# Performance work log

Measured on AMD Instinct MI355X. Metric: run time of the kernel, lower is better.

Reference implementation:

```python
import jax, jax.numpy as jnp
import numpy as np

B, T, D, H = 32, 1024, 512, 256  # bidirectional: hidden per direction = d_model // 2


def setup_inputs() -> dict:
    key = jax.random.key(0)
    ks = jax.random.split(key, 9)
    s = 1.0 / np.sqrt(H)  # torch default init scale
    return {
        "x": jax.random.normal(ks[0], (B, T, D), jnp.float32),
        "Wih_f": jax.random.normal(ks[1], (4 * H, D), jnp.float32) * s,
        "Whh_f": jax.random.normal(ks[2], (4 * H, H), jnp.float32) * s,
        "bih_f": jax.random.normal(ks[3], (4 * H,), jnp.float32) * s,
        "bhh_f": jax.random.normal(ks[4], (4 * H,), jnp.float32) * s,
        "Wih_b": jax.random.normal(ks[5], (4 * H, D), jnp.float32) * s,
        "Whh_b": jax.random.normal(ks[6], (4 * H, H), jnp.float32) * s,
        "bib_b": jax.random.normal(ks[7], (4 * H,), jnp.float32) * s,
        "bhh_b": jax.random.normal(ks[8], (4 * H,), jnp.float32) * s,
    }


def _lstm_dir(x, Wih, Whh, bih, bhh):
    # x: [B, T, D]; torch gate order: i, f, g, o
    b, t, _ = x.shape
    h_dim = Whh.shape[1]
    xp = jnp.einsum('btd,gd->btg', x, Wih) + bih + bhh  # [B, T, 4H]

    def step(carry, xt):
        h, c = carry
        gates = xt + h @ Whh.T  # [B, 4H]
        i, f, g, o = jnp.split(gates, 4, axis=-1)
        i = jax.nn.sigmoid(i)
        f = jax.nn.sigmoid(f)
        g = jnp.tanh(g)
        o = jax.nn.sigmoid(o)
        c = f * c + i * g
        h = o * jnp.tanh(c)
        return (h, c), h

    init = (jnp.zeros((b, h_dim), x.dtype), jnp.zeros((b, h_dim), x.dtype))
    _, hs = jax.lax.scan(step, init, jnp.swapaxes(xp, 0, 1))  # [T, B, H]
    return jnp.swapaxes(hs, 0, 1)  # [B, T, H]


def reference(x, Wih_f, Whh_f, bih_f, bhh_f, Wih_b, Whh_b, bib_b, bhh_b):
    # force_1d is identity for 3D input
    out_f = _lstm_dir(x, Wih_f, Whh_f, bih_f, bhh_f)
    out_b = _lstm_dir(x[:, ::-1, :], Wih_b, Whh_b, bib_b, bhh_b)[:, ::-1, :]
    return jnp.concatenate([out_f, out_b], axis=-1)  # [B, T, 2H] = [B, T, d_model]
```

## Files before the change

### kernel.cpp

```cpp
#include <hip/hip_runtime.h>
#include <cstdint>
#include <cstddef>


typedef unsigned int   uint;
typedef unsigned short ushort;

constexpr int Tn = 1024;
constexpr int Bn = 32;
constexpr int Dn = 512;
constexpr int Hn = 256;
constexpr int NC = 2048;
constexpr int KT = 512;

typedef _Float16 half8  __attribute__((ext_vector_type(8)));
typedef float    f32x4  __attribute__((ext_vector_type(4)));
typedef int      i32x4  __attribute__((ext_vector_type(4)));

__device__ __forceinline__ ushort f2h(float f) {
  _Float16 h = (_Float16)f;
  return __builtin_bit_cast(ushort, h);
}
__device__ __forceinline__ float h2f(ushort s) {
  return (float)__builtin_bit_cast(_Float16, s);
}
__device__ __forceinline__ uint packh(float a, float b) {
  return (uint)f2h(a) | ((uint)f2h(b) << 16);
}
__device__ __forceinline__ f32x4 mf(uint4 a, uint4 b, f32x4 c) {
  return __builtin_amdgcn_mfma_f32_16x16x32_f16(
      __builtin_bit_cast(half8, a), __builtin_bit_cast(half8, b), c, 0, 0, 0);
}
__device__ __forceinline__ i32x4 mfi8(uint4 a, uint4 b, i32x4 c) {
  return __builtin_amdgcn_mfma_i32_16x16x64_i8(
      __builtin_bit_cast(i32x4, a), __builtin_bit_cast(i32x4, b), c, 0, 0, 0);
}

__device__ __forceinline__ float sig_(float x) {
  x = fminf(fmaxf(x, -30.f), 30.f);
  return 1.f / (1.f + __expf(-x));
}
__device__ __forceinline__ float tanh_(float x) {
  x = fminf(fmaxf(x, -15.f), 15.f);
  float e = __expf(2.f * x);
  return (e - 1.f) / (e + 1.f);
}

__device__ __forceinline__ void barrier_lgkm() {
  asm volatile("s_waitcnt lgkmcnt(0)" ::: "memory");
  __builtin_amdgcn_s_barrier();
}


__global__ void k_prep_a(const float* __restrict__ x, ushort* __restrict__ a16, long nquad) {
  long i4 = (long)blockIdx.x * blockDim.x + threadIdx.x;
  if (i4 >= nquad) return;
  const float4 v = ((const float4*)x)[i4];
  ushort4 o;
  o.x = f2h(v.x); o.y = f2h(v.y); o.z = f2h(v.z); o.w = f2h(v.w);
  ((ushort4*)a16)[i4] = o;
}

__global__ void k_prep_w(const float* __restrict__ wf, const float* __restrict__ wb,
                         const float* __restrict__ bf1, const float* __restrict__ bf2,
                         const float* __restrict__ bb1, const float* __restrict__ bb2,
                         ushort* __restrict__ w16, float* __restrict__ biasc) {
  long i4 = (long)blockIdx.x * blockDim.x + threadIdx.x;
  if (i4 >= (long)NC * (KT / 4)) return;
  int n = (int)(i4 >> 7);
  int k4 = (int)(i4 & 127);
  int dir = n >> 10, g = n & 1023;
  const float* w = dir ? wb : wf;
  const float4 v = ((const float4*)(w + (size_t)g * Dn))[k4];
  ushort4 o;
  o.x = f2h(v.x); o.y = f2h(v.y); o.z = f2h(v.z); o.w = f2h(v.w);
  ((ushort4*)w16)[i4] = o;
  if (k4 == 0) biasc[n] = dir ? (bb1[g] + bb2[g]) : (bf1[g] + bf2[g]);
}

__global__ void k_scale(const float* __restrict__ whhF, const float* __restrict__ whhB,
                        float* __restrict__ sq) {
  int t = blockIdx.x * blockDim.x + threadIdx.x;
  if (t >= 2048) return;
  int dir = t >> 10, row = t & 1023;
  const float* w = (dir ? whhB : whhF) + (size_t)row * Hn;
  float m = 0.f;
  for (int i = 0; i < Hn; ++i) m = fmaxf(m, fabsf(w[i]));
  sq[t] = fmaxf(m, 1e-30f) / 127.f;
}

__global__ void k_prep_whh8(const float* __restrict__ whhF, const float* __restrict__ whhB,
                            const float* __restrict__ sq, uint4* __restrict__ WF8) {
  int t = blockIdx.x * blockDim.x + threadIdx.x;
  if (t >= 2 * 8 * 32 * 64) return;
  int lane = t & 63;
  int frag = (t >> 6) & 31;
  int w    = (t >> 11) & 7;
  int dir  = (t >> 14) & 1;
  int m  = frag & 7, kt = frag >> 3;
  int g = m >> 1, j = m & 1;
  int row = (g * 16 + 2 * w + j) * 16 + (lane & 15);
  int kb  = kt * 64 + (lane >> 4) * 16;
  const float* whh = dir ? whhB : whhF;
  const float* src = whh + (size_t)row * Hn + kb;
  float inv = 1.f / sq[dir * 1024 + row];
  uint pk[4];
#pragma unroll
  for (int q = 0; q < 4; ++q) {
    uint v = 0;
#pragma unroll
    for (int b = 0; b < 4; ++b) {
      float f = src[q * 4 + b] * inv;
      int iq = (int)rintf(fminf(fmaxf(f, -127.f), 127.f));
      v |= ((uint)(unsigned char)(signed char)iq) << (8 * b);
    }
    pk[q] = v;
  }
  WF8[t] = (uint4){pk[0], pk[1], pk[2], pk[3]};
}

__global__ void k_bad(float* __restrict__ out, int n) {
  int i = blockIdx.x * blockDim.x + threadIdx.x;
  if (i < n) out[i] = 54321.f;
}


__device__ __forceinline__ void gload_lds16(const void* g, void* l) {
  __builtin_amdgcn_global_load_lds((const __attribute__((address_space(1))) void*)g,
                                   (__attribute__((address_space(3))) void*)l, 16, 0, 0);
}

__global__ __launch_bounds__(256) void k_gemm(const ushort* __restrict__ A,
                                              const ushort* __restrict__ W,
                                              const float* __restrict__ biasc,
                                              ushort* __restrict__ xp) {
  __shared__ __align__(16) ushort As[128 * 32];
  __shared__ __align__(16) ushort Bs[128 * 32];
  const int bid = blockIdx.x;
  const int m0 = (bid >> 4) * 128;
  const int n0 = (bid & 15) * 128;
  const int tid = threadIdx.x;
  const int wid = tid >> 6, lane = tid & 63;
  const int wr = wid >> 1, wcq = wid & 1;
  const int l16 = lane & 15, lq = lane >> 4;

  f32x4 acc[4][4] = {};

  for (int kt = 0; kt < KT; kt += 32) {
    __syncthreads();
#pragma unroll
    for (int i = 0; i < 2; ++i) {
      int ch = wid * 2 + i;
      int p = ch * 64 + lane;
      int r = p >> 2, gp = p & 3;
      int gs = gp ^ ((r >> 1) & 3);
      gload_lds16(A + (size_t)(m0 + r) * KT + kt + gs * 8, (char*)As + ch * 1024);
      gload_lds16(W + (size_t)(n0 + r) * KT + kt + gs * 8, (char*)Bs + ch * 1024);
    }
    __syncthreads();

    half8 af[4], bfr[4];
#pragma unroll
    for (int mfi = 0; mfi < 4; ++mfi) {
      int row = wr * 64 + mfi * 16 + l16;
      int g = lq ^ ((row >> 1) & 3);
      af[mfi] = *(const half8*)((const char*)As + row * 64 + g * 16);
    }
#pragma unroll
    for (int nf = 0; nf < 4; ++nf) {
      int row = wcq * 64 + nf * 16 + l16;
      int g = lq ^ ((row >> 1) & 3);
      bfr[nf] = *(const half8*)((const char*)Bs + row * 64 + g * 16);
    }
#pragma unroll
    for (int mfi = 0; mfi < 4; ++mfi)
#pragma unroll
      for (int nf = 0; nf < 4; ++nf)
        acc[mfi][nf] = __builtin_amdgcn_mfma_f32_16x16x32_f16(af[mfi], bfr[nf], acc[mfi][nf], 0, 0, 0);
  }

#pragma unroll
  for (int nf = 0; nf < 4; ++nf) {
    int col = n0 + wcq * 64 + nf * 16 + l16;
    float bv = biasc[col];
#pragma unroll
    for (int mfi = 0; mfi < 4; ++mfi) {
      int rbase = m0 + wr * 64 + mfi * 16 + lq * 4;
#pragma unroll
      for (int i = 0; i < 4; ++i)
        xp[(size_t)(rbase + i) * NC + col] = f2h(acc[mfi][nf][i] + bv);
    }
  }
}


__global__ __launch_bounds__(512, 2) void k_lstm(const uint4* __restrict__ WF8,
                                                 const float* __restrict__ sq,
                                                 const ushort* __restrict__ xp,
                                                 float* __restrict__ out,
                                                 int b_base) {
  const int dir = blockIdx.x & 1;
  const int bl  = blockIdx.x >> 1;
  const int tid = threadIdx.x;
  const int w    = tid >> 6;
  const int lane = tid & 63;
  const int lq   = lane >> 4;
  const int n    = lane & 31;

  __shared__ __align__(16) char hq[2][256];
  __shared__ __align__(16) int  gbuf[8][128];

  const uint4* wfb = WF8 + (size_t)((dir * 8 + w) * 32) * 64 + lane;
  uint4 wA[32];
#pragma unroll
  for (int f = 0; f < 32; ++f) wA[f] = wfb[(size_t)f * 64];

  float fdq[4];
#pragma unroll
  for (int g = 0; g < 4; ++g)
    fdq[g] = sq[dir * 1024 + g * 256 + 32 * w + n] * (1.f / 127.f);

  if (tid < 128) ((uint*)hq)[tid] = 0;
  float creg = 0.f;
  __syncthreads();

  const int dstep = dir ? -1 : 1;
  const int t0 = dir ? (Tn - 1) : 0;
  const ptrdiff_t xstr = (ptrdiff_t)dstep * NC;
  const ptrdiff_t ostr = (ptrdiff_t)dstep * 512;
  const ushort* px = xp + (size_t)(bl * Tn + t0) * NC + dir * 1024 + 32 * w + n;
  float* pout = out + (size_t)((b_base + bl) * Tn + t0) * 512 + dir * 256 + 32 * w + n;

  int cur = 0;
#pragma unroll 1
  for (int t = 0; t < Tn; ++t) {
    ushort xg0 = px[0], xg1 = px[256], xg2 = px[512], xg3 = px[768];
    px += xstr;

    uint4 bq[4];
#pragma unroll
    for (int kt = 0; kt < 4; ++kt)
      bq[kt] = *(const uint4*)(hq[cur] + kt * 64 + lq * 16);

    i32x4 acc[8];
#pragma unroll
    for (int m = 0; m < 8; ++m) acc[m] = (i32x4){0, 0, 0, 0};
#pragma unroll
    for (int kt = 0; kt < 4; ++kt)
#pragma unroll
      for (int m = 0; m < 8; ++m)
        acc[m] = mfi8(wA[kt * 8 + m], bq[kt], acc[m]);

    if ((lane & 15) == 0) {
#pragma unroll
      for (int m = 0; m < 8; ++m)
        *(i32x4*)&gbuf[w][(m >> 1) * 32 + (m & 1) * 16 + lq * 4] = acc[m];
    }
    float gi = (float)gbuf[w][0 * 32 + n] * fdq[0] + h2f(xg0);
    float gf = (float)gbuf[w][1 * 32 + n] * fdq[1] + h2f(xg1);
    float gg = (float)gbuf[w][2 * 32 + n] * fdq[2] + h2f(xg2);
    float go = (float)gbuf[w][3 * 32 + n] * fdq[3] + h2f(xg3);
    float iv = sig_(gi), fv = sig_(gf), gv = tanh_(gg), ov = sig_(go);
    creg = fv * creg + iv * gv;
    float h = ov * tanh_(creg);
    if (lane < 32) {
      *pout = h;
      int q = (int)rintf(h * 127.f);
      hq[cur ^ 1][32 * w + n] = (char)q;
    }
    pout += ostr;
    barrier_lgkm();
    cur ^= 1;
  }
}


extern "C" void kernel_launch(void* const* d_in, const int* in_sizes, int n_in,
                              void* d_out, int out_size, void* d_ws, size_t ws_size,
                              hipStream_t stream) {
  const float* x     = (const float*)d_in[0];
  const float* Wih_f = (const float*)d_in[1];
  const float* Whh_f = (const float*)d_in[2];
  const float* bih_f = (const float*)d_in[3];
  const float* bhh_f = (const float*)d_in[4];
  const float* Wih_b = (const float*)d_in[5];
  const float* Whh_b = (const float*)d_in[6];
  const float* bib_b = (const float*)d_in[7];
  const float* bhh_b = (const float*)d_in[8];
  float* out = (float*)d_out;

  const size_t szW16  = (size_t)NC * KT * 2;
  const size_t szBias = (size_t)NC * 4;
  const size_t szSq   = 2048 * 4;
  const size_t szWF8  = (size_t)2 * 8 * 32 * 64 * 16;

  int c = 0;
  size_t szA16 = 0, szXp = 0;
  for (int cc = 1; cc <= 16; cc *= 2) {
    size_t a = (size_t)(Bn / cc) * Tn * KT * 2;
    size_t p = (size_t)(Bn / cc) * Tn * NC * 2;
    if (szW16 + szBias + szSq + szWF8 + a + p <= ws_size) { c = cc; szA16 = a; szXp = p; break; }
  }
  if (c == 0) {
    k_bad<<<(out_size + 255) / 256, 256, 0, stream>>>(out, out_size);
    return;
  }

  char* ws = (char*)d_ws;
  ushort* W16   = (ushort*)ws;
  float*  biasc = (float*)(ws + szW16);
  float*  sq    = (float*)(ws + szW16 + szBias);
  uint4*  WF8   = (uint4*)(ws + szW16 + szBias + szSq);
  ushort* A16   = (ushort*)(ws + szW16 + szBias + szSq + szWF8);
  ushort* xp    = (ushort*)(ws + szW16 + szBias + szSq + szWF8 + szA16);

  {
    long n4 = (long)NC * (KT / 4);
    k_prep_w<<<(int)((n4 + 255) / 256), 256, 0, stream>>>(Wih_f, Wih_b, bih_f, bhh_f,
                                                          bib_b, bhh_b, W16, biasc);
  }
  k_scale<<<8, 256, 0, stream>>>(Whh_f, Whh_b, sq);
  k_prep_whh8<<<(2 * 8 * 32 * 64) / 256, 256, 0, stream>>>(Whh_f, Whh_b, sq, WF8);

  const int sizeB = Bn / c;
  for (int cb = 0; cb < c; ++cb) {
    const int b_base = cb * sizeB;
    {
      long nquad = (long)sizeB * Tn * KT / 4;
      k_prep_a<<<(int)((nquad + 255) / 256), 256, 0, stream>>>(
          x + (size_t)b_base * Tn * Dn, A16, nquad);
    }
    k_gemm<<<dim3(sizeB * 8 * 16), dim3(256), 0, stream>>>(A16, W16, biasc, xp);
    k_lstm<<<dim3(2 * sizeB), dim3(512), 0, stream>>>(WF8, sq, xp, out, b_base);
  }
}
```

Before: 1.307 ms.

## Prefetch next-step xp gates, split MFMA chains, use fast reciprocal activations

Loads the next timestep's input-projection values one iteration ahead so their global-load latency overlaps the current step's recurrent MFMA work. It also splits the eight MFMA accumulators into two interleaved halves, storing the even half to LDS before issuing the odd half. Sigmoid and tanh now use a hardware reciprocal builtin without clamping. This trims latency on the serial per-timestep critical path, at the cost of slightly lower activation precision and possible inf handling at extreme inputs.

```diff
diff --git a/kernel.cpp b/kernel.cpp
--- a/kernel.cpp
+++ b/kernel.cpp
@@ -36,14 +36,25 @@
       __builtin_bit_cast(i32x4, a), __builtin_bit_cast(i32x4, b), c, 0, 0, 0);
 }
 
+#if defined(__has_builtin)
+#  if __has_builtin(__builtin_amdgcn_rcpf)
+#    define RCPF(x) __builtin_amdgcn_rcpf(x)
+#  endif
+#endif
+#ifndef RCPF
+#  define RCPF(x) (1.f / (x))
+#endif
+
+__device__ __forceinline__ float sigr_(float x) {
+  return RCPF(1.f + __expf(-x));
+}
+__device__ __forceinline__ float tanhr_(float x) {
+  float e = __expf(2.f * x);
+  return fmaf(-2.f, RCPF(e + 1.f), 1.f);
+}
 __device__ __forceinline__ float sig_(float x) {
   x = fminf(fmaxf(x, -30.f), 30.f);
   return 1.f / (1.f + __expf(-x));
-}
-__device__ __forceinline__ float tanh_(float x) {
-  x = fminf(fmaxf(x, -15.f), 15.f);
-  float e = __expf(2.f * x);
-  return (e - 1.f) / (e + 1.f);
 }
 
 __device__ __forceinline__ void barrier_lgkm() {
@@ -231,47 +242,65 @@
   const ushort* px = xp + (size_t)(bl * Tn + t0) * NC + dir * 1024 + 32 * w + n;
   float* pout = out + (size_t)((b_base + bl) * Tn + t0) * 512 + dir * 256 + 32 * w + n;
 
+  float xc0 = h2f(px[0]), xc1 = h2f(px[256]), xc2 = h2f(px[512]), xc3 = h2f(px[768]);
+
   int cur = 0;
 #pragma unroll 1
   for (int t = 0; t < Tn; ++t) {
-    ushort xg0 = px[0], xg1 = px[256], xg2 = px[512], xg3 = px[768];
-    px += xstr;
-
     uint4 bq[4];
 #pragma unroll
     for (int kt = 0; kt < 4; ++kt)
       bq[kt] = *(const uint4*)(hq[cur] + kt * 64 + lq * 16);
 
+    float xn0 = 0.f, xn1 = 0.f, xn2 = 0.f, xn3 = 0.f;
+    if (t + 1 < Tn) {
+      px += xstr;
+      xn0 = h2f(px[0]); xn1 = h2f(px[256]); xn2 = h2f(px[512]); xn3 = h2f(px[768]);
+    }
+
     i32x4 acc[8];
 #pragma unroll
     for (int m = 0; m < 8; ++m) acc[m] = (i32x4){0, 0, 0, 0};
+
 #pragma unroll
     for (int kt = 0; kt < 4; ++kt)
 #pragma unroll
-      for (int m = 0; m < 8; ++m)
+      for (int m = 0; m < 8; m += 2)
         acc[m] = mfi8(wA[kt * 8 + m], bq[kt], acc[m]);
-
     if ((lane & 15) == 0) {
 #pragma unroll
-      for (int m = 0; m < 8; ++m)
-        *(i32x4*)&gbuf[w][(m >> 1) * 32 + (m & 1) * 16 + lq * 4] = acc[m];
-    }
-    float gi = (float)gbuf[w][0 * 32 + n] * fdq[0] + h2f(xg0);
-    float gf = (float)gbuf[w][1 * 32 + n] * fdq[1] + h2f(xg1);
-    float gg = (float)gbuf[w][2 * 32 + n] * fdq[2] + h2f(xg2);
-    float go = (float)gbuf[w][3 * 32 + n] * fdq[3] + h2f(xg3);
-    float iv = sig_(gi), fv = sig_(gf), gv = tanh_(gg), ov = sig_(go);
+      for (int m = 0; m < 8; m += 2)
+        *(i32x4*)&gbuf[w][(m >> 1) * 32 + lq * 4] = acc[m];
+    }
+#pragma unroll
+    for (int kt = 0; kt < 4; ++kt)
+#pragma unroll
+      for (int m = 1; m < 8; m += 2)
+        acc[m] = mfi8(wA[kt * 8 + m], bq[kt], acc[m]);
+    if ((lane & 15) == 0) {
+#pragma unroll
+      for (int m = 1; m < 8; m += 2)
+        *(i32x4*)&gbuf[w][(m >> 1) * 32 + 16 + lq * 4] = acc[m];
+    }
+
+    float gi = (float)gbuf[w][0 * 32 + n] * fdq[0] + xc0;
+    float gf = (float)gbuf[w][1 * 32 + n] * fdq[1] + xc1;
+    float gg = (float)gbuf[w][2 * 32 + n] * fdq[2] + xc2;
+    float go = (float)gbuf[w][3 * 32 + n] * fdq[3] + xc3;
+    float iv = sigr_(gi), fv = sigr_(gf), gv = tanhr_(gg), ov = sigr_(go);
     creg = fv * creg + iv * gv;
-    float h = ov * tanh_(creg);
+    float h = ov * tanhr_(creg);
     if (lane < 32) {
       *pout = h;
       int q = (int)rintf(h * 127.f);
       hq[cur ^ 1][32 * w + n] = (char)q;
     }
     pout += ostr;
+    xc0 = xn0; xc1 = xn1; xc2 = xn2; xc3 = xn3;
     barrier_lgkm();
     cur ^= 1;
   }
+  (void)sig_;
 }
 
 
```

Result: faster. 1.279 ms (-2.2%).
